# Performance work log

Hardware: AMD Instinct MI355X
Metric: run time of the kernel (lower is better)

The kernel has to match this reference:

```python
import jax, jax.numpy as jnp
import numpy as np

IN_FEATURES = 4096
LOCAL_FEATURES = 32
KERNEL_SIZE = 64
STRIDE = 1
PADDING = KERNEL_SIZE - 1
FOLD_NUM = (IN_FEATURES + PADDING - KERNEL_SIZE) // STRIDE + 1  # = 4096
BATCH = 256


def setup_inputs() -> dict:
    key = jax.random.key(0)
    k_x, k_w = jax.random.split(key, 2)
    x = jax.random.normal(k_x, (BATCH, IN_FEATURES), dtype=jnp.float32)
    # xavier_uniform over (kernel_size, local_features) fan dims
    limit = float(np.sqrt(6.0 / (KERNEL_SIZE + LOCAL_FEATURES)))
    weight = jax.random.uniform(
        k_w, (FOLD_NUM, KERNEL_SIZE, LOCAL_FEATURES),
        dtype=jnp.float32, minval=-limit, maxval=limit)
    bias = jnp.zeros((FOLD_NUM, LOCAL_FEATURES), dtype=jnp.float32)
    return {"x": x, "weight": weight, "bias": bias}


def reference(x, weight, bias):
    # pad right by kernel_size-1 with zeros (F.pad([0, padding]))
    xp = jnp.pad(x, ((0, 0), (0, PADDING)))
    # unfold: windows[b, f, k] = xp[b, f*stride + k]
    idx = jnp.arange(FOLD_NUM)[:, None] * STRIDE + jnp.arange(KERNEL_SIZE)[None, :]
    windows = xp[:, idx]  # [B, fold_num, kernel_size]
    # per-position matmul with unique weights + bias
    out = jnp.einsum('bfk,fkl->bfl', windows, weight) + bias  # [B, fold_num, local_features]
    return out
```

## Files before the change

kernel.cpp:

```cpp
#include <hip/hip_runtime.h>
#include <hip/hip_bf16.h>

#define IN_FEATURES   4096
#define LOCAL_FEATURES  32
#define KERNEL_SIZE     64
#define FOLD_NUM      4096
#define BATCH          256

#define XROW 4192
#define KPAD 96

using bf16 = __hip_bfloat16;
typedef __attribute__((ext_vector_type(8))) short bf16x8;
typedef __attribute__((ext_vector_type(4))) float f32x4;

static __device__ __forceinline__ short bfbits(float v) {
    __hip_bfloat16 h = __float2bfloat16(v);
    return *reinterpret_cast<short*>(&h);
}

__global__ void convert_pad_x(const float* __restrict__ x, bf16* __restrict__ xb) {
    const int u   = blockIdx.x * 256 + threadIdx.x;
    const int row = u / 524;
    const int c8  = (u - row * 524) * 8;
    bf16x8 o;
    if (c8 < 4096) {
        const float4 a = *reinterpret_cast<const float4*>(x + (size_t)row * 4096 + c8);
        const float4 b = *reinterpret_cast<const float4*>(x + (size_t)row * 4096 + c8 + 4);
        o[0] = bfbits(a.x); o[1] = bfbits(a.y); o[2] = bfbits(a.z); o[3] = bfbits(a.w);
        o[4] = bfbits(b.x); o[5] = bfbits(b.y); o[6] = bfbits(b.z); o[7] = bfbits(b.w);
    } else {
        o = (bf16x8){0,0,0,0,0,0,0,0};
    }
    *reinterpret_cast<bf16x8*>(xb + (size_t)row * XROW + c8) = o;
}

__global__ void transpose_w(const float* __restrict__ w, bf16* __restrict__ wt) {
    __shared__ bf16 lds[2][32][KPAD];
    const int t  = threadIdx.x;
    const int f0 = blockIdx.x * 2;

    {
        uint4* z = reinterpret_cast<uint4*>(&lds[0][0][0]);
        const uint4 zz = {0, 0, 0, 0};
        z[t] = zz; z[t + 256] = zz; z[t + 512] = zz;
    }
    __syncthreads();

    {
        const int fp  = t >> 7;
        const int tt  = t & 127;
        const int shf = (f0 + fp) & 7;
        const float* src = w + (size_t)(f0 + fp) * 2048 + tt * 16;
        #pragma unroll
        for (int v = 0; v < 4; ++v) {
            const float4 val = *reinterpret_cast<const float4*>(src + v * 4);
            const int e  = tt * 16 + v * 4;
            const int k  = e >> 5;
            const int n0 = e & 31;
            lds[fp][n0 + 0][k + shf] = __float2bfloat16(val.x);
            lds[fp][n0 + 1][k + shf] = __float2bfloat16(val.y);
            lds[fp][n0 + 2][k + shf] = __float2bfloat16(val.z);
            lds[fp][n0 + 3][k + shf] = __float2bfloat16(val.w);
        }
    }
    __syncthreads();

    if (t < 192) {
        const int fp = t / 96;
        const int tt = t - fp * 96;
        const int n  = tt / 3;
        const int k0 = (tt - n * 3) * 32;
        const uint4* lp = reinterpret_cast<const uint4*>(&lds[fp][n][k0]);
        uint4* gp = reinterpret_cast<uint4*>(wt + ((size_t)(f0 + fp) * 32 + n) * KPAD + k0);
        gp[0] = lp[0]; gp[1] = lp[1]; gp[2] = lp[2]; gp[3] = lp[3];
    }
}

__global__ __launch_bounds__(256, 4)
void local_linear_main(const bf16* __restrict__ xb, const bf16* __restrict__ wt,
                       const float* __restrict__ bias, float* __restrict__ out)
{
    const int bid  = blockIdx.x;
    const int t    = threadIdx.x;
    const int lane = t & 63;
    const int wid  = t >> 6;

    const int fgrp  = (bid & 7) * 128 + (bid >> 6);
    const int btile = (bid >> 3) & 7;

    const int f     = fgrp * 4 + wid;
    const int base8 = f & ~7;
    const int lrow  = lane & 15;
    const int kgrp  = lane >> 4;
    const int b0    = btile * 32;

    const bf16* wbase = wt + (size_t)f * (32 * KPAD) + kgrp * 8;
    bf16x8 afr[2][3];
    #pragma unroll
    for (int mt = 0; mt < 2; ++mt)
        #pragma unroll
        for (int ks = 0; ks < 3; ++ks)
            afr[mt][ks] = *reinterpret_cast<const bf16x8*>(
                wbase + (mt * 16 + lrow) * KPAD + ks * 32);

    const bf16* xbase = xb + base8 + kgrp * 8;
    bf16x8 bfr[2][3];
    #pragma unroll
    for (int bt = 0; bt < 2; ++bt)
        #pragma unroll
        for (int ks = 0; ks < 3; ++ks)
            bfr[bt][ks] = *reinterpret_cast<const bf16x8*>(
                xbase + (size_t)(b0 + bt * 16 + lrow) * XROW + ks * 32);

    f32x4 acc[2][2];
    #pragma unroll
    for (int mt = 0; mt < 2; ++mt)
        #pragma unroll
        for (int bt = 0; bt < 2; ++bt)
            acc[mt][bt] = (f32x4){0.f, 0.f, 0.f, 0.f};

    #pragma unroll
    for (int ks = 0; ks < 3; ++ks)
        #pragma unroll
        for (int mt = 0; mt < 2; ++mt)
            #pragma unroll
            for (int bt = 0; bt < 2; ++bt)
                acc[mt][bt] = __builtin_amdgcn_mfma_f32_16x16x32_bf16(
                    afr[mt][ks], bfr[bt][ks], acc[mt][bt], 0, 0, 0);

    #pragma unroll
    for (int mt = 0; mt < 2; ++mt) {
        const float4 bv = *reinterpret_cast<const float4*>(
            bias + f * 32 + mt * 16 + kgrp * 4);
        #pragma unroll
        for (int bt = 0; bt < 2; ++bt) {
            const size_t b = b0 + bt * 16 + lrow;
            float4 o;
            o.x = acc[mt][bt][0] + bv.x;
            o.y = acc[mt][bt][1] + bv.y;
            o.z = acc[mt][bt][2] + bv.z;
            o.w = acc[mt][bt][3] + bv.w;
            *reinterpret_cast<float4*>(
                out + (b * FOLD_NUM + f) * 32 + mt * 16 + kgrp * 4) = o;
        }
    }
}

#define LDA 80
#define LDB 80
__global__ __launch_bounds__(256, 2)
void local_linear_kernel(const float* __restrict__ x, const float* __restrict__ w,
                         const float* __restrict__ bias, float* __restrict__ out)
{
    __shared__ bf16 As[BATCH * LDA];
    __shared__ bf16 Bs[LOCAL_FEATURES * LDB];
    const int f = blockIdx.x, t = threadIdx.x, lane = t & 63, wid = t >> 6;
    {
        const int col = lane, gcol = f + col;
        const bool valid = (gcol < IN_FEATURES);
        const float* xp = x + gcol;
        #pragma unroll 8
        for (int i = 0; i < 64; ++i) {
            const int row = wid + i * 4;
            float v = valid ? xp[(size_t)row * IN_FEATURES] : 0.0f;
            As[row * LDA + col] = __float2bfloat16(v);
        }
    }
    {
        const float* wf = w + (size_t)f * (KERNEL_SIZE * LOCAL_FEATURES);
        #pragma unroll
        for (int v4 = 0; v4 < 2; ++v4) {
            const int e0 = (t + v4 * 256) * 4;
            const float4 val = *reinterpret_cast<const float4*>(wf + e0);
            const int k = e0 >> 5, n = e0 & 31;
            Bs[(n + 0) * LDB + k] = __float2bfloat16(val.x);
            Bs[(n + 1) * LDB + k] = __float2bfloat16(val.y);
            Bs[(n + 2) * LDB + k] = __float2bfloat16(val.z);
            Bs[(n + 3) * LDB + k] = __float2bfloat16(val.w);
        }
    }
    __syncthreads();
    f32x4 acc[4][2];
    #pragma unroll
    for (int mt = 0; mt < 4; ++mt)
        #pragma unroll
        for (int nt = 0; nt < 2; ++nt) acc[mt][nt] = (f32x4){0.f,0.f,0.f,0.f};
    const int lrow = lane & 15, kgrp = lane >> 4;
    #pragma unroll
    for (int ks = 0; ks < 2; ++ks) {
        const int kbase = ks * 32 + kgrp * 8;
        bf16x8 bfrag[2], afrag[4];
        #pragma unroll
        for (int nt = 0; nt < 2; ++nt)
            bfrag[nt] = *reinterpret_cast<const bf16x8*>(&Bs[(nt*16+lrow) * LDB + kbase]);
        #pragma unroll
        for (int mt = 0; mt < 4; ++mt)
            afrag[mt] = *reinterpret_cast<const bf16x8*>(&As[(wid*64+mt*16+lrow) * LDA + kbase]);
        #pragma unroll
        for (int mt = 0; mt < 4; ++mt)
            #pragma unroll
            for (int nt = 0; nt < 2; ++nt)
                acc[mt][nt] = __builtin_amdgcn_mfma_f32_16x16x32_bf16(
                    afrag[mt], bfrag[nt], acc[mt][nt], 0, 0, 0);
    }
    float bv[2];
    bv[0] = bias[f * 32 + lrow];
    bv[1] = bias[f * 32 + 16 + lrow];
    #pragma unroll
    for (int mt = 0; mt < 4; ++mt)
        #pragma unroll
        for (int nt = 0; nt < 2; ++nt) {
            const int n = nt * 16 + lrow;
            #pragma unroll
            for (int r = 0; r < 4; ++r) {
                const int b = wid * 64 + mt * 16 + kgrp * 4 + r;
                out[((size_t)b * FOLD_NUM + f) * 32 + n] = acc[mt][nt][r] + bv[nt];
            }
        }
}

extern "C" void kernel_launch(void* const* d_in, const int* in_sizes, int n_in,
                              void* d_out, int out_size, void* d_ws, size_t ws_size,
                              hipStream_t stream) {
    const float* x    = (const float*)d_in[0];
    const float* wgt  = (const float*)d_in[1];
    const float* bias = (const float*)d_in[2];
    float* out        = (float*)d_out;

    const size_t WS_X = (size_t)BATCH * XROW * sizeof(bf16);
    const size_t WS_W = (size_t)FOLD_NUM * 32 * KPAD * sizeof(bf16);

    if (ws_size >= WS_X + WS_W) {
        bf16* xb = (bf16*)d_ws;
        bf16* wt = (bf16*)((char*)d_ws + WS_X);
        convert_pad_x<<<524, 256, 0, stream>>>(x, xb);
        transpose_w<<<FOLD_NUM / 2, 256, 0, stream>>>(wgt, wt);
        local_linear_main<<<8192, 256, 0, stream>>>(xb, wt, bias, out);
    } else {
        local_linear_kernel<<<FOLD_NUM, 256, 0, stream>>>(x, wgt, bias, out);
    }
}
```

Baseline: 203.0 us.

## Reuse x fragments across four fold positions per wave and merge prep kernels

The main kernel now has each wave compute four consecutive fold positions, reusing one set of x fragments from the 8-aligned window group, and the grid shrinks from 8192 to 2048 blocks. The x conversion and weight transpose kernels are fused into a single launch that splits work by block index. This aims to cut redundant x loads and one launch. In exchange, accumulator register pressure rises and there are fewer blocks to hide memory latency on a mostly write-bound kernel.

```diff
diff --git a/kernel.cpp b/kernel.cpp
--- a/kernel.cpp
+++ b/kernel.cpp
@@ -19,34 +19,35 @@
     return *reinterpret_cast<short*>(&h);
 }
 
-__global__ void convert_pad_x(const float* __restrict__ x, bf16* __restrict__ xb) {
-    const int u   = blockIdx.x * 256 + threadIdx.x;
-    const int row = u / 524;
-    const int c8  = (u - row * 524) * 8;
-    bf16x8 o;
-    if (c8 < 4096) {
-        const float4 a = *reinterpret_cast<const float4*>(x + (size_t)row * 4096 + c8);
-        const float4 b = *reinterpret_cast<const float4*>(x + (size_t)row * 4096 + c8 + 4);
-        o[0] = bfbits(a.x); o[1] = bfbits(a.y); o[2] = bfbits(a.z); o[3] = bfbits(a.w);
-        o[4] = bfbits(b.x); o[5] = bfbits(b.y); o[6] = bfbits(b.z); o[7] = bfbits(b.w);
-    } else {
-        o = (bf16x8){0,0,0,0,0,0,0,0};
-    }
-    *reinterpret_cast<bf16x8*>(xb + (size_t)row * XROW + c8) = o;
-}
-
-__global__ void transpose_w(const float* __restrict__ w, bf16* __restrict__ wt) {
+__global__ void prep_kernel(const float* __restrict__ x, const float* __restrict__ w,
+                            bf16* __restrict__ xb, bf16* __restrict__ wt) {
     __shared__ bf16 lds[2][32][KPAD];
-    const int t  = threadIdx.x;
+    const int t = threadIdx.x;
+
+    if (blockIdx.x >= 2048) {
+        const int u   = (blockIdx.x - 2048) * 256 + t;
+        const int row = u / 524;
+        const int c8  = (u - row * 524) * 8;
+        bf16x8 o;
+        if (c8 < 4096) {
+            const float4 a = *reinterpret_cast<const float4*>(x + (size_t)row * 4096 + c8);
+            const float4 b = *reinterpret_cast<const float4*>(x + (size_t)row * 4096 + c8 + 4);
+            o[0] = bfbits(a.x); o[1] = bfbits(a.y); o[2] = bfbits(a.z); o[3] = bfbits(a.w);
+            o[4] = bfbits(b.x); o[5] = bfbits(b.y); o[6] = bfbits(b.z); o[7] = bfbits(b.w);
+        } else {
+            o = (bf16x8){0,0,0,0,0,0,0,0};
+        }
+        *reinterpret_cast<bf16x8*>(xb + (size_t)row * XROW + c8) = o;
+        return;
+    }
+
     const int f0 = blockIdx.x * 2;
-
     {
         uint4* z = reinterpret_cast<uint4*>(&lds[0][0][0]);
         const uint4 zz = {0, 0, 0, 0};
         z[t] = zz; z[t + 256] = zz; z[t + 512] = zz;
     }
     __syncthreads();
-
     {
         const int fp  = t >> 7;
         const int tt  = t & 127;
@@ -65,7 +66,6 @@
         }
     }
     __syncthreads();
-
     if (t < 192) {
         const int fp = t / 96;
         const int tt = t - fp * 96;
@@ -77,72 +77,82 @@
     }
 }
 
-__global__ __launch_bounds__(256, 4)
+__global__ __launch_bounds__(256, 2)
 void local_linear_main(const bf16* __restrict__ xb, const bf16* __restrict__ wt,
                        const float* __restrict__ bias, float* __restrict__ out)
 {
-    const int bid  = blockIdx.x;
-    const int t    = threadIdx.x;
-    const int lane = t & 63;
-    const int wid  = t >> 6;
-
-    const int fgrp  = (bid & 7) * 128 + (bid >> 6);
-    const int btile = (bid >> 3) & 7;
-
-    const int f     = fgrp * 4 + wid;
-    const int base8 = f & ~7;
+    const int bid   = blockIdx.x;
+    const int t     = threadIdx.x;
+    const int lane  = t & 63;
+    const int wid   = t >> 6;
+
+    const int ftile = bid & 255;
+    const int btile = bid >> 8;
+    const int f0    = ftile * 16;
+    const int fw    = f0 + wid * 4;
+    const int base8 = fw & ~7;
     const int lrow  = lane & 15;
     const int kgrp  = lane >> 4;
     const int b0    = btile * 32;
 
-    const bf16* wbase = wt + (size_t)f * (32 * KPAD) + kgrp * 8;
-    bf16x8 afr[2][3];
-    #pragma unroll
-    for (int mt = 0; mt < 2; ++mt)
+    bf16x8 bfr[2][3];
+    {
+        const bf16* xbase = xb + base8 + kgrp * 8;
+        #pragma unroll
+        for (int bt = 0; bt < 2; ++bt)
+            #pragma unroll
+            for (int ks = 0; ks < 3; ++ks)
+                bfr[bt][ks] = *reinterpret_cast<const bf16x8*>(
+                    xbase + (size_t)(b0 + bt * 16 + lrow) * XROW + ks * 32);
+    }
+
+    f32x4 acc[4][2][2];
+    #pragma unroll
+    for (int i = 0; i < 4; ++i)
+        #pragma unroll
+        for (int mt = 0; mt < 2; ++mt)
+            #pragma unroll
+            for (int bt = 0; bt < 2; ++bt)
+                acc[i][mt][bt] = (f32x4){0.f, 0.f, 0.f, 0.f};
+
+    #pragma unroll
+    for (int i = 0; i < 4; ++i) {
+        const bf16* wbase = wt + (size_t)(fw + i) * (32 * KPAD) + kgrp * 8;
+        bf16x8 afr[2][3];
+        #pragma unroll
+        for (int mt = 0; mt < 2; ++mt)
+            #pragma unroll
+            for (int ks = 0; ks < 3; ++ks)
+                afr[mt][ks] = *reinterpret_cast<const bf16x8*>(
+                    wbase + (mt * 16 + lrow) * KPAD + ks * 32);
         #pragma unroll
         for (int ks = 0; ks < 3; ++ks)
-            afr[mt][ks] = *reinterpret_cast<const bf16x8*>(
-                wbase + (mt * 16 + lrow) * KPAD + ks * 32);
-
-    const bf16* xbase = xb + base8 + kgrp * 8;
-    bf16x8 bfr[2][3];
-    #pragma unroll
-    for (int bt = 0; bt < 2; ++bt)
-        #pragma unroll
-        for (int ks = 0; ks < 3; ++ks)
-            bfr[bt][ks] = *reinterpret_cast<const bf16x8*>(
-                xbase + (size_t)(b0 + bt * 16 + lrow) * XROW + ks * 32);
-
-    f32x4 acc[2][2];
-    #pragma unroll
-    for (int mt = 0; mt < 2; ++mt)
-        #pragma unroll
-        for (int bt = 0; bt < 2; ++bt)
-            acc[mt][bt] = (f32x4){0.f, 0.f, 0.f, 0.f};
-
-    #pragma unroll
-    for (int ks = 0; ks < 3; ++ks)
-        #pragma unroll
-        for (int mt = 0; mt < 2; ++mt)
-            #pragma unroll
-            for (int bt = 0; bt < 2; ++bt)
-                acc[mt][bt] = __builtin_amdgcn_mfma_f32_16x16x32_bf16(
-                    afr[mt][ks], bfr[bt][ks], acc[mt][bt], 0, 0, 0);
-
-    #pragma unroll
-    for (int mt = 0; mt < 2; ++mt) {
-        const float4 bv = *reinterpret_cast<const float4*>(
-            bias + f * 32 + mt * 16 + kgrp * 4);
-        #pragma unroll
-        for (int bt = 0; bt < 2; ++bt) {
-            const size_t b = b0 + bt * 16 + lrow;
-            float4 o;
-            o.x = acc[mt][bt][0] + bv.x;
-            o.y = acc[mt][bt][1] + bv.y;
-            o.z = acc[mt][bt][2] + bv.z;
-            o.w = acc[mt][bt][3] + bv.w;
-            *reinterpret_cast<float4*>(
-                out + (b * FOLD_NUM + f) * 32 + mt * 16 + kgrp * 4) = o;
+            #pragma unroll
+            for (int mt = 0; mt < 2; ++mt)
+                #pragma unroll
+                for (int bt = 0; bt < 2; ++bt)
+                    acc[i][mt][bt] = __builtin_amdgcn_mfma_f32_16x16x32_bf16(
+                        afr[mt][ks], bfr[bt][ks], acc[i][mt][bt], 0, 0, 0);
+    }
+
+    #pragma unroll
+    for (int i = 0; i < 4; ++i) {
+        const int f = fw + i;
+        #pragma unroll
+        for (int mt = 0; mt < 2; ++mt) {
+            const float4 bv = *reinterpret_cast<const float4*>(
+                bias + f * 32 + mt * 16 + kgrp * 4);
+            #pragma unroll
+            for (int bt = 0; bt < 2; ++bt) {
+                const size_t b = b0 + bt * 16 + lrow;
+                float4 o;
+                o.x = acc[i][mt][bt][0] + bv.x;
+                o.y = acc[i][mt][bt][1] + bv.y;
+                o.z = acc[i][mt][bt][2] + bv.z;
+                o.w = acc[i][mt][bt][3] + bv.w;
+                *reinterpret_cast<float4*>(
+                    out + (b * FOLD_NUM + f) * 32 + mt * 16 + kgrp * 4) = o;
+            }
         }
     }
 }
@@ -234,9 +244,8 @@
     if (ws_size >= WS_X + WS_W) {
         bf16* xb = (bf16*)d_ws;
         bf16* wt = (bf16*)((char*)d_ws + WS_X);
-        convert_pad_x<<<524, 256, 0, stream>>>(x, xb);
-        transpose_w<<<FOLD_NUM / 2, 256, 0, stream>>>(wgt, wt);
-        local_linear_main<<<8192, 256, 0, stream>>>(xb, wt, bias, out);
+        prep_kernel<<<2048 + 524, 256, 0, stream>>>(x, wgt, xb, wt);
+        local_linear_main<<<2048, 256, 0, stream>>>(xb, wt, bias, out);
     } else {
         local_linear_kernel<<<FOLD_NUM, 256, 0, stream>>>(x, wgt, bias, out);
     }
```

After: 193.6 us. 1.05x faster.
